# Kernel optimization log

Hardware: AMD Instinct MI355X
Metric: run time of the kernel (lower is better)

## Reference

```python
import jax, jax.numpy as jnp
import numpy as np

BN_EPS = 1e-5


def setup_inputs() -> dict:
    key = jax.random.key(0)
    ks = jax.random.split(key, 8)
    B, T, D, Tu, Dout, M = 32, 4096, 128, 512, 64, 8
    feats = jax.random.normal(ks[0], (B, T, D), dtype=jnp.float32)
    # integer time-window ids stored in channel 0 of x; pin 0 and Tu-1 so
    # tw_uniq = arange(0, Tu) exactly (no -99 padding) for every batch row
    tw = jax.random.randint(ks[1], (B, T), 0, Tu)
    tw = tw.at[:, 0].set(0).at[:, 1].set(Tu - 1)
    x = jnp.concatenate([tw[..., None].astype(jnp.float32), feats], axis=-1)
    mask = jax.random.uniform(ks[2], (B, T, 1)) < 0.9
    mask = mask.at[:, :2].set(True)  # keep pinned min/max entries valid
    tw_uniq = jnp.broadcast_to(jnp.arange(Tu, dtype=jnp.float32)[None, :, None], (B, Tu, 1))
    bn_gamma = jax.random.uniform(ks[3], (D,), jnp.float32, 0.5, 1.5)
    bn_beta = 0.1 * jax.random.normal(ks[4], (D,), dtype=jnp.float32)
    bn_mean = jnp.zeros((D,), jnp.float32)
    bn_var = jnp.ones((D,), jnp.float32)
    conv_w = jax.random.normal(ks[5], (Dout, D), dtype=jnp.float32) / np.float32(np.sqrt(D))
    conv_b = jnp.zeros((Dout,), jnp.float32)
    fc_w = jax.random.normal(ks[6], (M, Dout), dtype=jnp.float32) / np.float32(np.sqrt(Dout))
    fc_b = jnp.zeros((M,), jnp.float32)
    return dict(x=x, mask=mask, tw_uniq=tw_uniq, bn_gamma=bn_gamma, bn_beta=bn_beta,
                bn_mean=bn_mean, bn_var=bn_var, conv_w=conv_w, conv_b=conv_b,
                fc_w=fc_w, fc_b=fc_b)


def reference(x, mask, tw_uniq, bn_gamma, bn_beta, bn_mean, bn_var,
              conv_w, conv_b, fc_w, fc_b):
    # --- TimeWindowPooling (segment-max form of the dense expand+where+amax) ---
    # torch computes amax_T(where(tw==tw_uniq & mask, x, 0)) -> max(0, group max).
    # Equivalent: scatter-max of mask-zeroed values into a zeros-initialized
    # (B, Tu, D) buffer, avoiding the O(B*T*Tu*D) blowup.
    tw = x[..., 0]           # (B, T) integer-valued, detached in torch
    feats = x[..., 1:]       # (B, T, D)
    B, T, D = feats.shape
    Tu = tw_uniq.shape[1]
    u0 = tw_uniq[:, 0, 0]    # per-batch window minimum
    idx = jnp.clip((tw - u0[:, None]).astype(jnp.int32), 0, Tu - 1)  # (B, T)
    vals = jnp.where(mask, feats, 0.0)  # masked rows contribute 0 == init value
    hidden = jnp.zeros((B, Tu, D), feats.dtype).at[jnp.arange(B)[:, None], idx].max(vals)
    # --- mlp_down: BatchNorm1d (inference stats) + 1x1 Conv1d over channels ---
    h = (hidden - bn_mean) * jax.lax.rsqrt(bn_var + BN_EPS) * bn_gamma + bn_beta
    h = jnp.einsum('bud,od->buo', h, conv_w) + conv_b  # (B, Tu, Dout)
    # --- fc_out ---
    return jnp.einsum('buo,mo->bum', h, fc_w) + fc_b   # (B, Tu, M)
```

## Files before the change

kernel.cpp:

```cpp
#include <hip/hip_runtime.h>

#define B_   32
#define T_   4096
#define D_   128
#define TU   512
#define M_   8
#define O_   64
#define DCH  8
#define NCH  16
#define PAD  9
#define BN_EPS 1e-5f
#define UB   4

typedef float f4u __attribute__((ext_vector_type(4), aligned(4)));

#define WS_STRIDE (B_ * TU * M_)

__global__ __launch_bounds__(1024, 8) void fused_scatter_mm_kernel(
    const float* __restrict__ x,
    const int*   __restrict__ mask,
    const float* __restrict__ tw_uniq,
    const float* __restrict__ bn_gamma,
    const float* __restrict__ bn_beta,
    const float* __restrict__ bn_mean,
    const float* __restrict__ bn_var,
    const float* __restrict__ conv_w,
    const float* __restrict__ conv_b,
    const float* __restrict__ fc_w,
    const float* __restrict__ fc_b,
    float*       __restrict__ ws) {
    __shared__ unsigned hid[TU * PAD];
    __shared__ int uidxs[T_];
    __shared__ float wsm[M_ * DCH];
    __shared__ float tmp[M_ * DCH];
    __shared__ float biasc[M_];
    const int i = blockIdx.x;
    const int b = (i & 7) + 8 * ((i >> 3) & 3);
    const int c = i >> 5;
    const int tid = threadIdx.x;

    const float* xb = x + (size_t)b * T_ * (D_ + 1);
    const int*   mb = mask + b * T_;
    const float  u0 = tw_uniq[b * TU];

    for (int p = tid; p < TU * PAD; p += 1024) hid[p] = 0u;
#pragma unroll
    for (int k = 0; k < T_ / 1024; ++k) {
        const int t = k * 1024 + tid;
        const float twf = xb[(size_t)t * (D_ + 1)];
        const int   mk  = mb[t];
        const int   u   = min(max((int)(twf - u0), 0), TU - 1);
        uidxs[t] = mk ? u : -1;
    }
    if (tid < M_ * DCH) {
        const int m = tid >> 3, dl = tid & (DCH - 1), d = c * DCH + dl;
        float wraw = 0.f;
        for (int o = 0; o < O_; ++o) wraw += fc_w[m * O_ + o] * conv_w[o * D_ + d];
        const float sc = bn_gamma[d] * rsqrtf(bn_var[d] + BN_EPS);
        const float sh = bn_beta[d] - bn_mean[d] * sc;
        wsm[tid] = wraw * sc;
        tmp[tid] = wraw * sh;
    }
    __syncthreads();
    if (tid < M_) {
        float s = 0.f;
#pragma unroll
        for (int d = 0; d < DCH; ++d) s += tmp[tid * DCH + d];
        if (c == 0) {
            s += fc_b[tid];
            for (int o = 0; o < O_; ++o) s += fc_w[tid * O_ + o] * conv_b[o];
        }
        biasc[tid] = s;
    }

    const int q = tid & 1;
    const int r = tid >> 1;
    for (int it = 0; it < T_ / 512 / UB; ++it) {
        f4u fv[UB];
        int uu[UB];
#pragma unroll
        for (int j = 0; j < UB; ++j) {
            const int t = (it * UB + j) * 512 + r;
            fv[j] = *(const f4u*)(xb + (size_t)t * (D_ + 1) + 1 + c * DCH + q * 4);
        }
#pragma unroll
        for (int j = 0; j < UB; ++j) {
            uu[j] = uidxs[(it * UB + j) * 512 + r];
        }
#pragma unroll
        for (int j = 0; j < UB; ++j) {
            if (uu[j] >= 0) {
                unsigned* hp = &hid[uu[j] * PAD + q * 4];
                if (fv[j].x > 0.0f) atomicMax(hp + 0, __float_as_uint(fv[j].x));
                if (fv[j].y > 0.0f) atomicMax(hp + 1, __float_as_uint(fv[j].y));
                if (fv[j].z > 0.0f) atomicMax(hp + 2, __float_as_uint(fv[j].z));
                if (fv[j].w > 0.0f) atomicMax(hp + 3, __float_as_uint(fv[j].w));
            }
        }
    }
    __syncthreads();

    const int u  = tid & (TU - 1);
    const int mh = tid >> 9;
    float a0 = biasc[mh * 4 + 0];
    float a1 = biasc[mh * 4 + 1];
    float a2 = biasc[mh * 4 + 2];
    float a3 = biasc[mh * 4 + 3];
#pragma unroll
    for (int d = 0; d < DCH; ++d) {
        float h = __uint_as_float(hid[u * PAD + d]);
        a0 += h * wsm[(mh * 4 + 0) * DCH + d];
        a1 += h * wsm[(mh * 4 + 1) * DCH + d];
        a2 += h * wsm[(mh * 4 + 2) * DCH + d];
        a3 += h * wsm[(mh * 4 + 3) * DCH + d];
    }
    float4 av = make_float4(a0, a1, a2, a3);
    float* wp = ws + (size_t)c * WS_STRIDE + ((size_t)(b * TU + u)) * M_ + mh * 4;
    *(float4*)wp = av;
}

__global__ __launch_bounds__(256) void reduce_kernel(
    const float* __restrict__ ws, float* __restrict__ out) {
    const int j = blockIdx.x;
    const int s = j >> 3;
    const int b = (j & 7) + 8 * (s & 3);
    const int uc = s >> 2;
    const int idx = (b * TU + uc * 32) * M_ + threadIdx.x;
    float acc = 0.f;
#pragma unroll
    for (int c = 0; c < NCH; ++c) acc += ws[(size_t)c * WS_STRIDE + idx];
    out[idx] = acc;
}

extern "C" void kernel_launch(void* const* d_in, const int* in_sizes, int n_in,
                              void* d_out, int out_size, void* d_ws, size_t ws_size,
                              hipStream_t stream) {
    const float* x        = (const float*)d_in[0];
    const int*   mask     = (const int*)  d_in[1];
    const float* tw_uniq  = (const float*)d_in[2];
    const float* bn_gamma = (const float*)d_in[3];
    const float* bn_beta  = (const float*)d_in[4];
    const float* bn_mean  = (const float*)d_in[5];
    const float* bn_var   = (const float*)d_in[6];
    const float* conv_w   = (const float*)d_in[7];
    const float* conv_b   = (const float*)d_in[8];
    const float* fc_w     = (const float*)d_in[9];
    const float* fc_b     = (const float*)d_in[10];
    float* ws  = (float*)d_ws;
    float* out = (float*)d_out;

    fused_scatter_mm_kernel<<<512, 1024, 0, stream>>>(
        x, mask, tw_uniq, bn_gamma, bn_beta, bn_mean, bn_var,
        conv_w, conv_b, fc_w, fc_b, ws);
    reduce_kernel<<<512, 256, 0, stream>>>(ws, out);
}
```

Baseline: 139.0 us.

## Replace LDS atomic scatter-max with CSR bucket build and per-window gather-max

The LDS atomicMax scatter over 16 channel chunks, plus its cross-chunk reduce kernel, is replaced by a three-kernel pipeline. The first kernel computes window indices, the second builds per-batch CSR buckets with a counting sort, and the third has each wavefront gather the rows of one window, take the max, and apply the folded BN/conv/fc projection with shuffle reductions. This removes atomic contention and the partial-sum workspace round trip, and lets every block cover all 128 channels. In exchange it adds two extra launches and an irregular, data-dependent row gather. Within a bucket the gather is serial, so throughput rests on memory-level parallelism, and only 256 blocks are launched.

```diff
diff --git a/kernel.cpp b/kernel.cpp
--- a/kernel.cpp
+++ b/kernel.cpp
@@ -6,54 +6,88 @@
 #define TU   512
 #define M_   8
 #define O_   64
-#define DCH  8
-#define NCH  16
-#define PAD  9
 #define BN_EPS 1e-5f
-#define UB   4
 
 typedef float f4u __attribute__((ext_vector_type(4), aligned(4)));
 
-#define WS_STRIDE (B_ * TU * M_)
+#define WS_UIDX   0
+#define WS_BASE   (B_ * T_)
+#define WS_END    (WS_BASE + B_ * TU)
+#define WS_ROWIDX (WS_END + B_ * TU)
 
-__global__ __launch_bounds__(1024, 8) void fused_scatter_mm_kernel(
+
+__global__ __launch_bounds__(256) void index_kernel(
+    const float* __restrict__ x, const int* __restrict__ mask,
+    const float* __restrict__ tw_uniq, int* __restrict__ wsI) {
+    const int g = blockIdx.x * 256 + threadIdx.x;
+    const int b = g >> 12;
+    const float twf = x[(size_t)g * (D_ + 1)];
+    const int   mk  = mask[g];
+    const float u0  = tw_uniq[b * TU];
+    const int   u   = min(max((int)(twf - u0), 0), TU - 1);
+    wsI[WS_UIDX + g] = mk ? u : -1;
+}
+
+__global__ __launch_bounds__(1024) void build_kernel(int* __restrict__ wsI) {
+    __shared__ int cnt[TU];
+    __shared__ int scn[TU];
+    __shared__ int cur[TU];
+    const int b = blockIdx.x;
+    const int tid = threadIdx.x;
+    if (tid < TU) cnt[tid] = 0;
+    __syncthreads();
+    const int* ub = wsI + WS_UIDX + b * T_;
+    int uv[4];
+#pragma unroll
+    for (int r = 0; r < 4; ++r) {
+        uv[r] = ub[r * 1024 + tid];
+        if (uv[r] >= 0) atomicAdd(&cnt[uv[r]], 1);
+    }
+    __syncthreads();
+    if (tid < TU) scn[tid] = cnt[tid];
+    __syncthreads();
+    for (int off = 1; off < TU; off <<= 1) {
+        int v = 0;
+        if (tid < TU && tid >= off) v = scn[tid - off];
+        __syncthreads();
+        if (tid < TU) scn[tid] += v;
+        __syncthreads();
+    }
+    if (tid < TU) {
+        const int e = scn[tid];
+        const int s = e - cnt[tid];
+        wsI[WS_BASE + b * TU + tid] = s;
+        wsI[WS_END  + b * TU + tid] = e;
+        cur[tid] = s;
+    }
+    __syncthreads();
+    int* rb = wsI + WS_ROWIDX + b * T_;
+#pragma unroll
+    for (int r = 0; r < 4; ++r) {
+        if (uv[r] >= 0) {
+            const int pos = atomicAdd(&cur[uv[r]], 1);
+            rb[pos] = r * 1024 + tid;
+        }
+    }
+}
+
+__global__ __launch_bounds__(1024) void gather_mm_kernel(
     const float* __restrict__ x,
-    const int*   __restrict__ mask,
-    const float* __restrict__ tw_uniq,
-    const float* __restrict__ bn_gamma,
-    const float* __restrict__ bn_beta,
-    const float* __restrict__ bn_mean,
-    const float* __restrict__ bn_var,
-    const float* __restrict__ conv_w,
-    const float* __restrict__ conv_b,
-    const float* __restrict__ fc_w,
-    const float* __restrict__ fc_b,
-    float*       __restrict__ ws) {
-    __shared__ unsigned hid[TU * PAD];
-    __shared__ int uidxs[T_];
-    __shared__ float wsm[M_ * DCH];
-    __shared__ float tmp[M_ * DCH];
+    const float* __restrict__ bn_gamma, const float* __restrict__ bn_beta,
+    const float* __restrict__ bn_mean,  const float* __restrict__ bn_var,
+    const float* __restrict__ conv_w,   const float* __restrict__ conv_b,
+    const float* __restrict__ fc_w,     const float* __restrict__ fc_b,
+    const int* __restrict__ wsI, float* __restrict__ out) {
+    __shared__ float wsm[M_ * D_];
+    __shared__ float tmp[M_ * D_];
     __shared__ float biasc[M_];
-    const int i = blockIdx.x;
-    const int b = (i & 7) + 8 * ((i >> 3) & 3);
-    const int c = i >> 5;
+    const int j = blockIdx.x;
+    const int b  = (j & 7) + 8 * ((j >> 3) & 3);
+    const int uc = j >> 5;
     const int tid = threadIdx.x;
 
-    const float* xb = x + (size_t)b * T_ * (D_ + 1);
-    const int*   mb = mask + b * T_;
-    const float  u0 = tw_uniq[b * TU];
-
-    for (int p = tid; p < TU * PAD; p += 1024) hid[p] = 0u;
-#pragma unroll
-    for (int k = 0; k < T_ / 1024; ++k) {
-        const int t = k * 1024 + tid;
-        const float twf = xb[(size_t)t * (D_ + 1)];
-        const int   mk  = mb[t];
-        const int   u   = min(max((int)(twf - u0), 0), TU - 1);
-        uidxs[t] = mk ? u : -1;
-    }
-    if (tid < M_ * DCH) {
-        const int m = tid >> 3, dl = tid & (DCH - 1), d = c * DCH + dl;
+    {
+        const int m = tid >> 7, d = tid & (D_ - 1);
         float wraw = 0.f;
         for (int o = 0; o < O_; ++o) wraw += fc_w[m * O_ + o] * conv_w[o * D_ + d];
         const float sc = bn_gamma[d] * rsqrtf(bn_var[d] + BN_EPS);
@@ -63,73 +97,61 @@
     }
     __syncthreads();
     if (tid < M_) {
-        float s = 0.f;
-#pragma unroll
-        for (int d = 0; d < DCH; ++d) s += tmp[tid * DCH + d];
-        if (c == 0) {
-            s += fc_b[tid];
-            for (int o = 0; o < O_; ++o) s += fc_w[tid * O_ + o] * conv_b[o];
-        }
+        float s = fc_b[tid];
+        for (int o = 0; o < O_; ++o) s += fc_w[tid * O_ + o] * conv_b[o];
+        for (int d = 0; d < D_; ++d) s += tmp[tid * D_ + d];
         biasc[tid] = s;
-    }
-
-    const int q = tid & 1;
-    const int r = tid >> 1;
-    for (int it = 0; it < T_ / 512 / UB; ++it) {
-        f4u fv[UB];
-        int uu[UB];
-#pragma unroll
-        for (int j = 0; j < UB; ++j) {
-            const int t = (it * UB + j) * 512 + r;
-            fv[j] = *(const f4u*)(xb + (size_t)t * (D_ + 1) + 1 + c * DCH + q * 4);
-        }
-#pragma unroll
-        for (int j = 0; j < UB; ++j) {
-            uu[j] = uidxs[(it * UB + j) * 512 + r];
-        }
-#pragma unroll
-        for (int j = 0; j < UB; ++j) {
-            if (uu[j] >= 0) {
-                unsigned* hp = &hid[uu[j] * PAD + q * 4];
-                if (fv[j].x > 0.0f) atomicMax(hp + 0, __float_as_uint(fv[j].x));
-                if (fv[j].y > 0.0f) atomicMax(hp + 1, __float_as_uint(fv[j].y));
-                if (fv[j].z > 0.0f) atomicMax(hp + 2, __float_as_uint(fv[j].z));
-                if (fv[j].w > 0.0f) atomicMax(hp + 3, __float_as_uint(fv[j].w));
-            }
-        }
     }
     __syncthreads();
 
-    const int u  = tid & (TU - 1);
-    const int mh = tid >> 9;
-    float a0 = biasc[mh * 4 + 0];
-    float a1 = biasc[mh * 4 + 1];
-    float a2 = biasc[mh * 4 + 2];
-    float a3 = biasc[mh * 4 + 3];
+    const int w    = tid >> 6;
+    const int lane = tid & 63;
+    const int half = lane >> 5;
+    const int lq   = lane & 31;
+    const float* xb = x + (size_t)b * T_ * (D_ + 1);
+    const int* rowb = wsI + WS_ROWIDX + b * T_;
+
+    for (int k = 0; k < 4; ++k) {
+        const int u = uc * 64 + w * 4 + k;
+        const int start = wsI[WS_BASE + b * TU + u];
+        const int end   = wsI[WS_END  + b * TU + u];
+        float a0 = 0.f, a1 = 0.f, a2 = 0.f, a3 = 0.f;
+        int  r    = start + half;
+        bool have = r < end;
+        f4u  vn;
+        if (have) { vn = *(const f4u*)(xb + (size_t)rowb[r] * (D_ + 1) + 1 + lq * 4); r += 2; }
+        while (have) {
+            const f4u v = vn;
+            have = r < end;
+            if (have) { vn = *(const f4u*)(xb + (size_t)rowb[r] * (D_ + 1) + 1 + lq * 4); r += 2; }
+            a0 = fmaxf(a0, v.x); a1 = fmaxf(a1, v.y);
+            a2 = fmaxf(a2, v.z); a3 = fmaxf(a3, v.w);
+        }
+        a0 = fmaxf(a0, __shfl_xor(a0, 32)); a1 = fmaxf(a1, __shfl_xor(a1, 32));
+        a2 = fmaxf(a2, __shfl_xor(a2, 32)); a3 = fmaxf(a3, __shfl_xor(a3, 32));
+
+        const int db = lq * 4;
+        float p0, p1, p2, p3, p4, p5, p6, p7;
+#define PDOT(mm) (a0 * wsm[(mm) * D_ + db] + a1 * wsm[(mm) * D_ + db + 1] + \
+                  a2 * wsm[(mm) * D_ + db + 2] + a3 * wsm[(mm) * D_ + db + 3])
+        p0 = PDOT(0); p1 = PDOT(1); p2 = PDOT(2); p3 = PDOT(3);
+        p4 = PDOT(4); p5 = PDOT(5); p6 = PDOT(6); p7 = PDOT(7);
+#undef PDOT
 #pragma unroll
-    for (int d = 0; d < DCH; ++d) {
-        float h = __uint_as_float(hid[u * PAD + d]);
-        a0 += h * wsm[(mh * 4 + 0) * DCH + d];
-        a1 += h * wsm[(mh * 4 + 1) * DCH + d];
-        a2 += h * wsm[(mh * 4 + 2) * DCH + d];
-        a3 += h * wsm[(mh * 4 + 3) * DCH + d];
+        for (int off = 1; off < 32; off <<= 1) {
+            p0 += __shfl_xor(p0, off); p1 += __shfl_xor(p1, off);
+            p2 += __shfl_xor(p2, off); p3 += __shfl_xor(p3, off);
+            p4 += __shfl_xor(p4, off); p5 += __shfl_xor(p5, off);
+            p6 += __shfl_xor(p6, off); p7 += __shfl_xor(p7, off);
+        }
+        if (lane == 0) {
+            float* op = out + ((size_t)(b * TU + u)) * M_;
+            *(float4*)(op)     = make_float4(p0 + biasc[0], p1 + biasc[1],
+                                             p2 + biasc[2], p3 + biasc[3]);
+            *(float4*)(op + 4) = make_float4(p4 + biasc[4], p5 + biasc[5],
+                                             p6 + biasc[6], p7 + biasc[7]);
+        }
     }
-    float4 av = make_float4(a0, a1, a2, a3);
-    float* wp = ws + (size_t)c * WS_STRIDE + ((size_t)(b * TU + u)) * M_ + mh * 4;
-    *(float4*)wp = av;
-}
-
-__global__ __launch_bounds__(256) void reduce_kernel(
-    const float* __restrict__ ws, float* __restrict__ out) {
-    const int j = blockIdx.x;
-    const int s = j >> 3;
-    const int b = (j & 7) + 8 * (s & 3);
-    const int uc = s >> 2;
-    const int idx = (b * TU + uc * 32) * M_ + threadIdx.x;
-    float acc = 0.f;
-#pragma unroll
-    for (int c = 0; c < NCH; ++c) acc += ws[(size_t)c * WS_STRIDE + idx];
-    out[idx] = acc;
 }
 
 extern "C" void kernel_launch(void* const* d_in, const int* in_sizes, int n_in,
@@ -146,11 +168,12 @@
     const float* conv_b   = (const float*)d_in[8];
     const float* fc_w     = (const float*)d_in[9];
     const float* fc_b     = (const float*)d_in[10];
-    float* ws  = (float*)d_ws;
+    int*   wsI = (int*)d_ws;
     float* out = (float*)d_out;
 
-    fused_scatter_mm_kernel<<<512, 1024, 0, stream>>>(
-        x, mask, tw_uniq, bn_gamma, bn_beta, bn_mean, bn_var,
-        conv_w, conv_b, fc_w, fc_b, ws);
-    reduce_kernel<<<512, 256, 0, stream>>>(ws, out);
+    index_kernel<<<512, 256, 0, stream>>>(x, mask, tw_uniq, wsI);
+    build_kernel<<<32, 1024, 0, stream>>>(wsI);
+    gather_mm_kernel<<<256, 1024, 0, stream>>>(
+        x, bn_gamma, bn_beta, bn_mean, bn_var,
+        conv_w, conv_b, fc_w, fc_b, wsI, out);
 }
```

New measurement: 141.6 us. About the same (+1.8%).
